# Optimization experiments

Hardware: AMD Instinct MI355X
Metric: run time of the kernel (lower is better)

The kernel has to match this reference:

```python
import jax, jax.numpy as jnp
import numpy as np
from jax import lax

B, T, D, H = 64, 512, 512, 512


def setup_inputs() -> dict:
    key = jax.random.key(0)
    k1, k2, k3, k4 = jax.random.split(key, 4)
    inputs = jax.random.normal(k1, (B, T, D), dtype=jnp.float32)
    lengths = jax.random.randint(k2, (B,), 1, T + 1, dtype=jnp.int32)
    c0 = jnp.zeros((B, H), dtype=jnp.float32)
    h0 = jnp.zeros((B, H), dtype=jnp.float32)
    scale_i = 1.0 / np.sqrt(D)
    scale_h = 1.0 / np.sqrt(H)
    Wi = jax.random.normal(k3, (D, 4 * H), dtype=jnp.float32) * scale_i
    Wh = jax.random.normal(k4, (H, 4 * H), dtype=jnp.float32) * scale_h
    b = jnp.zeros((4 * H,), dtype=jnp.float32)
    return {"inputs": inputs, "lengths": lengths, "c0": c0, "h0": h0,
            "Wi": Wi, "Wh": Wh, "b": b, "reverse": 1}


def _flip_sequences(seq, lengths):
    # seq: [B, T, F]; keeps padding at the end while flipping valid prefix.
    t = seq.shape[1]
    idxs = (jnp.arange(t - 1, -1, -1)[None, :] + lengths[:, None]) % t  # [B, T]
    return jnp.take_along_axis(seq, idxs[:, :, None], axis=1)


def reference(inputs, lengths, c0, h0, Wi, Wh, b, reverse):
    batch, t, _ = inputs.shape
    if reverse:
        inputs = _flip_sequences(inputs, lengths)

    def step(carry, x_t):
        c, h = carry
        z = x_t @ Wi + h @ Wh + b  # [B, 4H]
        i_g, f_g, g_g, o_g = jnp.split(z, 4, axis=-1)
        c_new = jax.nn.sigmoid(f_g) * c + jax.nn.sigmoid(i_g) * jnp.tanh(g_g)
        h_new = jax.nn.sigmoid(o_g) * jnp.tanh(c_new)
        return (c_new, h_new), (c_new, h_new)

    xs = jnp.swapaxes(inputs, 0, 1)  # [T, B, D]
    _, (cs, hs) = lax.scan(step, (c0, h0), xs)
    cs = jnp.swapaxes(cs, 0, 1)  # [B, T, H]
    hs = jnp.swapaxes(hs, 0, 1)  # [B, T, H]
    outputs = hs

    last = lengths - 1
    bidx = jnp.arange(batch)
    c_final = cs[bidx, last]
    h_final = hs[bidx, last]

    if reverse:
        outputs = _flip_sequences(outputs, lengths)
    return outputs, (c_final, h_final)
```

## Files before the change

### kernel.cpp

```cpp
#include <hip/hip_runtime.h>

#define B_ 64
#define T_ 512
#define D_ 512
#define H_ 512
#define NG 2048

typedef __attribute__((ext_vector_type(8))) short short8;
typedef __attribute__((ext_vector_type(4))) float floatx4;

static __device__ __forceinline__ unsigned short f2bf(float f) {
    unsigned int u = __float_as_uint(f);
    return (unsigned short)((u + 0x7FFFu + ((u >> 16) & 1u)) >> 16);
}

static __device__ __forceinline__ short8 pack8(float4 a, float4 b) {
    short8 r;
    r[0] = (short)f2bf(a.x); r[1] = (short)f2bf(a.y);
    r[2] = (short)f2bf(a.z); r[3] = (short)f2bf(a.w);
    r[4] = (short)f2bf(b.x); r[5] = (short)f2bf(b.y);
    r[6] = (short)f2bf(b.z); r[7] = (short)f2bf(b.w);
    return r;
}

static __device__ __forceinline__ float sigm(float x) { return 1.0f / (1.0f + __expf(-x)); }
static __device__ __forceinline__ float tanh_(float x) {
    float e = __expf(2.0f * x);
    return 1.0f - 2.0f / (e + 1.0f);
}

__global__ __launch_bounds__(256) void transpose_w(
    const float* __restrict__ Wi, const float* __restrict__ Wh,
    unsigned short* __restrict__ WiT, unsigned short* __restrict__ WhT)
{
    __shared__ float tile[64][65];
    const float* src = blockIdx.z ? Wh : Wi;
    unsigned short* dst = blockIdx.z ? WhT : WiT;
    const int n0 = blockIdx.x * 64, k0 = blockIdx.y * 64;
    const int cx = threadIdx.x & 63, ry = threadIdx.x >> 6;
#pragma unroll
    for (int i = 0; i < 16; ++i) {
        int k = ry * 16 + i;
        tile[k][cx] = src[(size_t)(k0 + k) * NG + n0 + cx];
    }
    __syncthreads();
#pragma unroll
    for (int i = 0; i < 16; ++i) {
        int n = ry * 16 + i;
        dst[(size_t)(n0 + n) * D_ + k0 + cx] = f2bf(tile[cx][n]);
    }
}

__global__ __launch_bounds__(256) void zx_gemm(
    const float* __restrict__ x, const int* __restrict__ lengths,
    const unsigned short* __restrict__ WiT, const float* __restrict__ bias,
    const int* __restrict__ revp, _Float16* __restrict__ zx)
{
    __shared__ unsigned short a_lds[128][40];
    __shared__ unsigned short b_lds[128][40];

    const int mt = blockIdx.x, nt = blockIdx.y;
    const int tid = threadIdx.x;
    const int lane = tid & 63, w = tid >> 6;
    const int wm = w & 1, wn = w >> 1;

    const int b = mt >> 2;
    const int len = lengths[b];
    const int rev = revp[0];

    const int r = tid >> 1;
    const int kh = (tid & 1) << 4;
    const int t = ((mt & 3) << 7) + r;
    const int src_t = rev ? ((T_ - 1 - t + len) & (T_ - 1)) : t;
    const float* arow = x + ((size_t)b * T_ + src_t) * D_;
    const unsigned short* brow = WiT + (size_t)(nt * 128 + r) * D_;

    floatx4 acc[4][4];
#pragma unroll
    for (int i = 0; i < 4; ++i)
#pragma unroll
        for (int j = 0; j < 4; ++j) acc[i][j] = (floatx4){0.f, 0.f, 0.f, 0.f};

    for (int kt = 0; kt < D_ / 32; ++kt) {
        const float4* ap = (const float4*)(arow + kt * 32 + kh);
        float4 a0 = ap[0], a1 = ap[1], a2 = ap[2], a3 = ap[3];
        const uint4* bp = (const uint4*)(brow + kt * 32 + kh);
        uint4 bq0 = bp[0], bq1 = bp[1];
        *(short8*)&a_lds[r][kh]     = pack8(a0, a1);
        *(short8*)&a_lds[r][kh + 8] = pack8(a2, a3);
        *(uint4*)&b_lds[r][kh]     = bq0;
        *(uint4*)&b_lds[r][kh + 8] = bq1;
        __syncthreads();

        short8 af[4], bfr[4];
#pragma unroll
        for (int mi = 0; mi < 4; ++mi)
            af[mi] = *(const short8*)&a_lds[wm * 64 + mi * 16 + (lane & 15)][(lane >> 4) << 3];
#pragma unroll
        for (int ni = 0; ni < 4; ++ni)
            bfr[ni] = *(const short8*)&b_lds[wn * 64 + ni * 16 + (lane & 15)][(lane >> 4) << 3];
#pragma unroll
        for (int mi = 0; mi < 4; ++mi)
#pragma unroll
            for (int ni = 0; ni < 4; ++ni)
                acc[mi][ni] = __builtin_amdgcn_mfma_f32_16x16x32_bf16(af[mi], bfr[ni], acc[mi][ni], 0, 0, 0);
        __syncthreads();
    }

#pragma unroll
    for (int mi = 0; mi < 4; ++mi) {
#pragma unroll
        for (int ni = 0; ni < 4; ++ni) {
            int row = wm * 64 + mi * 16 + ((lane >> 4) << 2);
            int col = nt * 128 + wn * 64 + ni * 16 + (lane & 15);
            float bv = bias[col];
            size_t base = (size_t)(mt * 128 + row) * NG + col;
#pragma unroll
            for (int v = 0; v < 4; ++v)
                zx[base + (size_t)v * NG] = (_Float16)(acc[mi][ni][v] + bv);
        }
    }
}

__global__ __launch_bounds__(512, 2) void lstm_rec(
    const _Float16* __restrict__ zx, const unsigned short* __restrict__ WhT,
    const float* __restrict__ c0, const float* __restrict__ h0,
    const int* __restrict__ lengths, const int* __restrict__ revp,
    float* __restrict__ out, unsigned short* __restrict__ h_state,
    unsigned int* __restrict__ flags)
{
    __shared__ unsigned short h_lds[16][520];
    __shared__ float zred[8][8][256];
    __shared__ unsigned short h_next[8][64];

    const int bid = blockIdx.x;
    const int gb = bid & 7, gh = bid >> 3;
    const int tid = threadIdx.x;
    const int lane = tid & 63, w = tid >> 6;
    const int b0 = gb * 8, u0 = gh * 64;
    const int rev = revp[0];

    for (int i = tid; i < 8 * 520; i += 512)
        h_lds[8 + i / 520][i % 520] = 0;

    const int bi = tid >> 6;
    const int jj = tid & 63;
    const int len_b = lengths[b0 + bi];
    float c = c0[(size_t)(b0 + bi) * H_ + u0 + jj];

    short8 bw[16][2];
    const int colh = lane & 15;
    const int khw = (lane >> 4) << 3;
#pragma unroll
    for (int ni = 0; ni < 16; ++ni) {
        const int l = ni * 16 + colh;
        const unsigned short* src =
            WhT + (size_t)((l >> 6) * H_ + u0 + (l & 63)) * D_ + w * 64 + khw;
        bw[ni][0] = *(const short8*)(src);
        bw[ni][1] = *(const short8*)(src + 32);
    }

    float zxv[4];
    {
        const _Float16* zp = zx + ((size_t)(b0 + bi) * T_) * NG + u0 + jj;
#pragma unroll
        for (int g = 0; g < 4; ++g) zxv[g] = (float)zp[g * H_];
    }

    const int sr = tid >> 6;
    const int sc = (tid & 63) << 3;

    for (int s = 0; s < T_; ++s) {
        if (s == 0) {
            const float4* hp = (const float4*)(h0 + (size_t)(b0 + sr) * H_ + sc);
            float4 v0 = hp[0], v1 = hp[1];
            *(short8*)&h_lds[sr][sc] = pack8(v0, v1);
        } else {
            const unsigned long long* hp =
                (const unsigned long long*)(h_state + ((size_t)(s & 1) * B_ + b0 + sr) * H_ + sc);
            unsigned long long v0 = __hip_atomic_load(hp,     __ATOMIC_RELAXED, __HIP_MEMORY_SCOPE_AGENT);
            unsigned long long v1 = __hip_atomic_load(hp + 1, __ATOMIC_RELAXED, __HIP_MEMORY_SCOPE_AGENT);
            *(unsigned long long*)&h_lds[sr][sc]     = v0;
            *(unsigned long long*)&h_lds[sr][sc + 4] = v1;
        }
        __syncthreads();

        floatx4 acc[16];
#pragma unroll
        for (int ni = 0; ni < 16; ++ni) acc[ni] = (floatx4){0.f, 0.f, 0.f, 0.f};
        {
            const int arow = lane & 15;
#pragma unroll
            for (int kk = 0; kk < 2; ++kk) {
                short8 af = *(const short8*)&h_lds[arow][w * 64 + kk * 32 + khw];
#pragma unroll
                for (int ni = 0; ni < 16; ++ni)
                    acc[ni] = __builtin_amdgcn_mfma_f32_16x16x32_bf16(af, bw[ni][kk], acc[ni], 0, 0, 0);
            }
        }
        {
            const int rr = (lane >> 4) << 2;
            if (rr < 8) {
#pragma unroll
                for (int ni = 0; ni < 16; ++ni)
#pragma unroll
                    for (int v = 0; v < 4; ++v)
                        zred[w][rr + v][ni * 16 + colh] = acc[ni][v];
            }
        }
        __syncthreads();

        {
            float z[4];
#pragma unroll
            for (int g = 0; g < 4; ++g) {
                float a = zxv[g];
#pragma unroll
                for (int w2 = 0; w2 < 8; ++w2) a += zred[w2][bi][g * 64 + jj];
                z[g] = a;
            }
            float ig = sigm(z[0]), fg = sigm(z[1]);
            float gg = tanh_(z[2]), og = sigm(z[3]);
            float cn = fg * c + ig * gg;
            float hn = og * tanh_(cn);
            c = cn;
            int orig_t = rev ? ((T_ - 1 - s + len_b) & (T_ - 1)) : s;
            out[((size_t)(b0 + bi) * T_ + orig_t) * H_ + u0 + jj] = hn;
            h_next[bi][jj] = f2bf(hn);
            if (s == len_b - 1) {
                size_t fin = (size_t)B_ * T_ * H_;
                out[fin + (size_t)(b0 + bi) * H_ + u0 + jj] = cn;
                out[fin + (size_t)B_ * H_ + (size_t)(b0 + bi) * H_ + u0 + jj] = hn;
            }
        }
        __syncthreads();

        if (s + 1 < T_) {
            if (tid < 256) {
                const int bi2 = tid >> 5, j2 = (tid & 31) << 1;
                unsigned int val = (unsigned int)h_next[bi2][j2] |
                                   ((unsigned int)h_next[bi2][j2 + 1] << 16);
                unsigned short* dst =
                    h_state + ((size_t)((s + 1) & 1) * B_ + b0 + bi2) * H_ + u0 + j2;
                __hip_atomic_store((unsigned int*)dst, val, __ATOMIC_RELAXED, __HIP_MEMORY_SCOPE_AGENT);
            }
            {
                const _Float16* zp = zx + ((size_t)(b0 + bi) * T_ + (s + 1)) * NG + u0 + jj;
#pragma unroll
                for (int g = 0; g < 4; ++g) zxv[g] = (float)zp[g * H_];
            }
            __syncthreads();
            if (tid == 0) {
                __hip_atomic_fetch_add(&flags[s * 8 + gb], 1u, __ATOMIC_RELAXED, __HIP_MEMORY_SCOPE_AGENT);
                while (__hip_atomic_load(&flags[s * 8 + gb], __ATOMIC_RELAXED, __HIP_MEMORY_SCOPE_AGENT) < 8u)
                    __builtin_amdgcn_s_sleep(1);
            }
            __syncthreads();
        }
    }
}

extern "C" void kernel_launch(void* const* d_in, const int* in_sizes, int n_in,
                              void* d_out, int out_size, void* d_ws, size_t ws_size,
                              hipStream_t stream)
{
    const float* x       = (const float*)d_in[0];
    const int*   lengths = (const int*)d_in[1];
    const float* c0      = (const float*)d_in[2];
    const float* h0      = (const float*)d_in[3];
    const float* Wi      = (const float*)d_in[4];
    const float* Wh      = (const float*)d_in[5];
    const float* bias    = (const float*)d_in[6];
    const int*   revp    = (const int*)d_in[7];
    float* out = (float*)d_out;

    char* ws = (char*)d_ws;
    const size_t OFF_WIT = 0;
    const size_t OFF_WHT = 2ull << 20;
    const size_t OFF_ZX  = 4ull << 20;
    const size_t OFF_H   = OFF_ZX + (size_t)B_ * T_ * NG * 2;
    const size_t OFF_FLG = OFF_H + 2ull * B_ * H_ * 2;
    const size_t NEED    = OFF_FLG + (size_t)T_ * 8 * 4;
    if (ws_size < NEED) return;

    unsigned short* WiT = (unsigned short*)(ws + OFF_WIT);
    unsigned short* WhT = (unsigned short*)(ws + OFF_WHT);
    _Float16* zx        = (_Float16*)(ws + OFF_ZX);
    unsigned short* h_state = (unsigned short*)(ws + OFF_H);
    unsigned int* flags = (unsigned int*)(ws + OFF_FLG);

    hipMemsetAsync(flags, 0, (size_t)T_ * 8 * 4, stream);
    dim3 gt(32, 8, 2);
    transpose_w<<<gt, 256, 0, stream>>>(Wi, Wh, WiT, WhT);
    dim3 g1(256, 16);
    zx_gemm<<<g1, 256, 0, stream>>>(x, lengths, WiT, bias, revp, zx);
    lstm_rec<<<64, 512, 0, stream>>>(zx, WhT, c0, h0, lengths, revp, out, h_state, flags);
}
```

Before: 1.712 ms.

## Replace flag barrier with step-tagged h publication and split-N recurrent MFMA

Restructures the recurrent kernel so each of 64 blocks (256 threads) owns 16 batch rows and 32 hidden units and computes the full K=512 reduction per wave, which removes the LDS cross-wave reduction buffer. The per-step counter barrier is replaced by packing each bf16 h value with its step index into a 32-bit word, so consumers spin until every word they read carries the expected tag. Gate values are paired across lanes with a shuffle. This removes two block barriers and the global flag round-trip per step. In exchange, every consumer thread polls the data words directly, and the published h buffer doubles in size.

```diff
diff --git a/kernel.cpp b/kernel.cpp
--- a/kernel.cpp
+++ b/kernel.cpp
@@ -122,141 +122,144 @@
     }
 }
 
-__global__ __launch_bounds__(512, 2) void lstm_rec(
+__global__ __launch_bounds__(256, 1) void lstm_rec(
     const _Float16* __restrict__ zx, const unsigned short* __restrict__ WhT,
     const float* __restrict__ c0, const float* __restrict__ h0,
     const int* __restrict__ lengths, const int* __restrict__ revp,
-    float* __restrict__ out, unsigned short* __restrict__ h_state,
-    unsigned int* __restrict__ flags)
+    float* __restrict__ out, unsigned int* __restrict__ h_pub)
 {
     __shared__ unsigned short h_lds[16][520];
-    __shared__ float zred[8][8][256];
-    __shared__ unsigned short h_next[8][64];
 
     const int bid = blockIdx.x;
-    const int gb = bid & 7, gh = bid >> 3;
+    const int gb = bid & 3, gh = bid >> 2;
     const int tid = threadIdx.x;
     const int lane = tid & 63, w = tid >> 6;
-    const int b0 = gb * 8, u0 = gh * 64;
+    const int b0 = gb * 16, u0 = gh * 32;
     const int rev = revp[0];
 
-    for (int i = tid; i < 8 * 520; i += 512)
-        h_lds[8 + i / 520][i % 520] = 0;
-
-    const int bi = tid >> 6;
-    const int jj = tid & 63;
-    const int len_b = lengths[b0 + bi];
-    float c = c0[(size_t)(b0 + bi) * H_ + u0 + jj];
+    const int colh = lane & 15;
+    const int rr = (lane >> 4) << 2;
+    const int cg = colh >> 3;
+    const int cu = colh & 7;
+    const int uu = w * 8 + cu;
+    const int khw = (lane >> 4) << 3;
+
+    int len_v[4]; float c[4];
+#pragma unroll
+    for (int v = 0; v < 4; ++v) {
+        len_v[v] = lengths[b0 + rr + v];
+        c[v] = c0[(size_t)(b0 + rr + v) * H_ + u0 + uu];
+    }
 
     short8 bw[16][2];
-    const int colh = lane & 15;
-    const int khw = (lane >> 4) << 3;
-#pragma unroll
-    for (int ni = 0; ni < 16; ++ni) {
-        const int l = ni * 16 + colh;
-        const unsigned short* src =
-            WhT + (size_t)((l >> 6) * H_ + u0 + (l & 63)) * D_ + w * 64 + khw;
-        bw[ni][0] = *(const short8*)(src);
-        bw[ni][1] = *(const short8*)(src + 32);
-    }
-
-    float zxv[4];
-    {
-        const _Float16* zp = zx + ((size_t)(b0 + bi) * T_) * NG + u0 + jj;
-#pragma unroll
-        for (int g = 0; g < 4; ++g) zxv[g] = (float)zp[g * H_];
-    }
-
-    const int sr = tid >> 6;
-    const int sc = (tid & 63) << 3;
+#pragma unroll
+    for (int ni = 0; ni < 2; ++ni) {
+        const unsigned short* src = WhT + (size_t)((ni * 2 + cg) * H_ + u0 + uu) * D_ + khw;
+#pragma unroll
+        for (int kk = 0; kk < 16; ++kk)
+            bw[kk][ni] = *(const short8*)(src + kk * 32);
+    }
+
+    float zxv[2][4];
+#pragma unroll
+    for (int ni = 0; ni < 2; ++ni)
+#pragma unroll
+        for (int v = 0; v < 4; ++v)
+            zxv[ni][v] = (float)zx[((size_t)(b0 + rr + v) * T_) * NG + (ni * 2 + cg) * H_ + u0 + uu];
+
+    const int sr = tid >> 4;
+    const int scc = (tid & 15) << 5;
 
     for (int s = 0; s < T_; ++s) {
         if (s == 0) {
-            const float4* hp = (const float4*)(h0 + (size_t)(b0 + sr) * H_ + sc);
-            float4 v0 = hp[0], v1 = hp[1];
-            *(short8*)&h_lds[sr][sc] = pack8(v0, v1);
+            const float* hp = h0 + (size_t)(b0 + sr) * H_ + scc;
+#pragma unroll
+            for (int q = 0; q < 4; ++q) {
+                float4 f0 = *(const float4*)(hp + q * 8);
+                float4 f1 = *(const float4*)(hp + q * 8 + 4);
+                *(short8*)&h_lds[sr][scc + q * 8] = pack8(f0, f1);
+            }
         } else {
-            const unsigned long long* hp =
-                (const unsigned long long*)(h_state + ((size_t)(s & 1) * B_ + b0 + sr) * H_ + sc);
-            unsigned long long v0 = __hip_atomic_load(hp,     __ATOMIC_RELAXED, __HIP_MEMORY_SCOPE_AGENT);
-            unsigned long long v1 = __hip_atomic_load(hp + 1, __ATOMIC_RELAXED, __HIP_MEMORY_SCOPE_AGENT);
-            *(unsigned long long*)&h_lds[sr][sc]     = v0;
-            *(unsigned long long*)&h_lds[sr][sc + 4] = v1;
+            const unsigned int* src = h_pub + ((size_t)(s & 1) * B_ + b0 + sr) * H_ + scc;
+#pragma unroll
+            for (int half = 0; half < 2; ++half) {
+                const unsigned int* sp = src + half * 16;
+                unsigned int dwv[16];
+                for (;;) {
+                    bool ok = true;
+#pragma unroll
+                    for (int j = 0; j < 16; ++j)
+                        dwv[j] = __hip_atomic_load(sp + j, __ATOMIC_RELAXED, __HIP_MEMORY_SCOPE_AGENT);
+#pragma unroll
+                    for (int j = 0; j < 16; ++j)
+                        ok &= ((dwv[j] >> 16) == (unsigned)s);
+                    if (ok) break;
+                    __builtin_amdgcn_s_sleep(1);
+                }
+                short8 p0, p1;
+#pragma unroll
+                for (int j = 0; j < 8; ++j) {
+                    p0[j] = (short)(dwv[j] & 0xffffu);
+                    p1[j] = (short)(dwv[j + 8] & 0xffffu);
+                }
+                *(short8*)&h_lds[sr][scc + half * 16]     = p0;
+                *(short8*)&h_lds[sr][scc + half * 16 + 8] = p1;
+            }
         }
         __syncthreads();
 
-        floatx4 acc[16];
-#pragma unroll
-        for (int ni = 0; ni < 16; ++ni) acc[ni] = (floatx4){0.f, 0.f, 0.f, 0.f};
-        {
-            const int arow = lane & 15;
-#pragma unroll
-            for (int kk = 0; kk < 2; ++kk) {
-                short8 af = *(const short8*)&h_lds[arow][w * 64 + kk * 32 + khw];
-#pragma unroll
-                for (int ni = 0; ni < 16; ++ni)
-                    acc[ni] = __builtin_amdgcn_mfma_f32_16x16x32_bf16(af, bw[ni][kk], acc[ni], 0, 0, 0);
+        floatx4 acc[2];
+        acc[0] = (floatx4){0.f, 0.f, 0.f, 0.f};
+        acc[1] = (floatx4){0.f, 0.f, 0.f, 0.f};
+#pragma unroll
+        for (int kk = 0; kk < 16; ++kk) {
+            short8 af = *(const short8*)&h_lds[lane & 15][kk * 32 + khw];
+            acc[0] = __builtin_amdgcn_mfma_f32_16x16x32_bf16(af, bw[kk][0], acc[0], 0, 0, 0);
+            acc[1] = __builtin_amdgcn_mfma_f32_16x16x32_bf16(af, bw[kk][1], acc[1], 0, 0, 0);
+        }
+
+#pragma unroll
+        for (int v = 0; v < 4; ++v) {
+            float own0 = acc[0][v] + zxv[0][v];
+            float own1 = acc[1][v] + zxv[1][v];
+            float oth0 = __shfl_xor(own0, 8);
+            float oth1 = __shfl_xor(own1, 8);
+            float zi = cg ? oth0 : own0;
+            float zf = cg ? own0 : oth0;
+            float zg = cg ? oth1 : own1;
+            float zo = cg ? own1 : oth1;
+            float ig = sigm(zi), fg = sigm(zf);
+            float gg = tanh_(zg), og = sigm(zo);
+            float cn = fg * c[v] + ig * gg;
+            float hn = og * tanh_(cn);
+            c[v] = cn;
+
+            const int b = b0 + rr + v;
+            const int ug = u0 + uu;
+            int orig_t = rev ? ((T_ - 1 - s + len_v[v]) & (T_ - 1)) : s;
+            if (cg == 0)
+                out[((size_t)b * T_ + orig_t) * H_ + ug] = hn;
+            else if (s + 1 < T_) {
+                unsigned int val = (unsigned int)f2bf(hn) | ((unsigned int)(s + 1) << 16);
+                __hip_atomic_store(h_pub + ((size_t)((s + 1) & 1) * B_ + b) * H_ + ug, val,
+                                   __ATOMIC_RELAXED, __HIP_MEMORY_SCOPE_AGENT);
             }
-        }
-        {
-            const int rr = (lane >> 4) << 2;
-            if (rr < 8) {
-#pragma unroll
-                for (int ni = 0; ni < 16; ++ni)
-#pragma unroll
-                    for (int v = 0; v < 4; ++v)
-                        zred[w][rr + v][ni * 16 + colh] = acc[ni][v];
+            if (s == len_v[v] - 1) {
+                size_t fin = (size_t)B_ * T_ * H_;
+                if (cg == 0) out[fin + (size_t)b * H_ + ug] = cn;
+                else         out[fin + (size_t)B_ * H_ + (size_t)b * H_ + ug] = hn;
             }
         }
+
+        if (s + 1 < T_) {
+#pragma unroll
+            for (int ni = 0; ni < 2; ++ni)
+#pragma unroll
+                for (int v = 0; v < 4; ++v)
+                    zxv[ni][v] = (float)zx[((size_t)(b0 + rr + v) * T_ + s + 1) * NG +
+                                           (ni * 2 + cg) * H_ + u0 + uu];
+        }
         __syncthreads();
-
-        {
-            float z[4];
-#pragma unroll
-            for (int g = 0; g < 4; ++g) {
-                float a = zxv[g];
-#pragma unroll
-                for (int w2 = 0; w2 < 8; ++w2) a += zred[w2][bi][g * 64 + jj];
-                z[g] = a;
-            }
-            float ig = sigm(z[0]), fg = sigm(z[1]);
-            float gg = tanh_(z[2]), og = sigm(z[3]);
-            float cn = fg * c + ig * gg;
-            float hn = og * tanh_(cn);
-            c = cn;
-            int orig_t = rev ? ((T_ - 1 - s + len_b) & (T_ - 1)) : s;
-            out[((size_t)(b0 + bi) * T_ + orig_t) * H_ + u0 + jj] = hn;
-            h_next[bi][jj] = f2bf(hn);
-            if (s == len_b - 1) {
-                size_t fin = (size_t)B_ * T_ * H_;
-                out[fin + (size_t)(b0 + bi) * H_ + u0 + jj] = cn;
-                out[fin + (size_t)B_ * H_ + (size_t)(b0 + bi) * H_ + u0 + jj] = hn;
-            }
-        }
-        __syncthreads();
-
-        if (s + 1 < T_) {
-            if (tid < 256) {
-                const int bi2 = tid >> 5, j2 = (tid & 31) << 1;
-                unsigned int val = (unsigned int)h_next[bi2][j2] |
-                                   ((unsigned int)h_next[bi2][j2 + 1] << 16);
-                unsigned short* dst =
-                    h_state + ((size_t)((s + 1) & 1) * B_ + b0 + bi2) * H_ + u0 + j2;
-                __hip_atomic_store((unsigned int*)dst, val, __ATOMIC_RELAXED, __HIP_MEMORY_SCOPE_AGENT);
-            }
-            {
-                const _Float16* zp = zx + ((size_t)(b0 + bi) * T_ + (s + 1)) * NG + u0 + jj;
-#pragma unroll
-                for (int g = 0; g < 4; ++g) zxv[g] = (float)zp[g * H_];
-            }
-            __syncthreads();
-            if (tid == 0) {
-                __hip_atomic_fetch_add(&flags[s * 8 + gb], 1u, __ATOMIC_RELAXED, __HIP_MEMORY_SCOPE_AGENT);
-                while (__hip_atomic_load(&flags[s * 8 + gb], __ATOMIC_RELAXED, __HIP_MEMORY_SCOPE_AGENT) < 8u)
-                    __builtin_amdgcn_s_sleep(1);
-            }
-            __syncthreads();
-        }
     }
 }
 
@@ -278,21 +281,20 @@
     const size_t OFF_WIT = 0;
     const size_t OFF_WHT = 2ull << 20;
     const size_t OFF_ZX  = 4ull << 20;
-    const size_t OFF_H   = OFF_ZX + (size_t)B_ * T_ * NG * 2;
-    const size_t OFF_FLG = OFF_H + 2ull * B_ * H_ * 2;
-    const size_t NEED    = OFF_FLG + (size_t)T_ * 8 * 4;
+    const size_t OFF_HP  = OFF_ZX + (size_t)B_ * T_ * NG * 2;
+    const size_t HP_BYTES = 2ull * B_ * H_ * 4;
+    const size_t NEED    = OFF_HP + HP_BYTES;
     if (ws_size < NEED) return;
 
     unsigned short* WiT = (unsigned short*)(ws + OFF_WIT);
     unsigned short* WhT = (unsigned short*)(ws + OFF_WHT);
     _Float16* zx        = (_Float16*)(ws + OFF_ZX);
-    unsigned short* h_state = (unsigned short*)(ws + OFF_H);
-    unsigned int* flags = (unsigned int*)(ws + OFF_FLG);
-
-    hipMemsetAsync(flags, 0, (size_t)T_ * 8 * 4, stream);
+    unsigned int* h_pub = (unsigned int*)(ws + OFF_HP);
+
+    hipMemsetAsync(h_pub, 0, HP_BYTES, stream);
     dim3 gt(32, 8, 2);
     transpose_w<<<gt, 256, 0, stream>>>(Wi, Wh, WiT, WhT);
     dim3 g1(256, 16);
     zx_gemm<<<g1, 256, 0, stream>>>(x, lengths, WiT, bias, revp, zx);
-    lstm_rec<<<64, 512, 0, stream>>>(zx, WhT, c0, h0, lengths, revp, out, h_state, flags);
-}
+    lstm_rec<<<64, 256, 0, stream>>>(zx, WhT, c0, h0, lengths, revp, out, h_pub);
+}
```

After: 3.300 ms. +92.7%, slower.
